# Optimization experiments

Measured on AMD Instinct MI355X. Metric: run time of the kernel, lower is better.

Reference implementation:

```python
import jax, jax.numpy as jnp
import numpy as np
from jax import lax

ALPHA = 0.5       # voxel vs structure weighting
BETA = 0.5        # split vs merge weighting
THRESHOLD = 0.0   # logit threshold for binarizing predictions
N_ITERS = 48      # label-propagation + pointer-jumping rounds (effective reach ~2^N)


def _shift(x, axis, s):
    """Shift x by s along axis, zero-filling the boundary (labels are >= 0)."""
    pads = [(0, 0)] * x.ndim
    pads[axis] = (max(s, 0), max(-s, 0))
    xp = jnp.pad(x, pads)
    idx = [slice(None)] * x.ndim
    idx[axis] = slice(max(-s, 0), max(-s, 0) + x.shape[axis])
    return xp[tuple(idx)]


def label_ccl(mask):
    """Connected-component labeling of a 3D boolean mask with 6-connectivity
    (scipy.ndimage.label default structure). Each component ends up holding the
    max linear index (+1) of its voxels; background is 0. Uses max-propagation
    over the 6-neighborhood plus pointer jumping for fast convergence."""
    size = mask.size
    ids = jnp.arange(1, size + 1, dtype=jnp.int32).reshape(mask.shape)
    lbl0 = jnp.where(mask, ids, 0)

    def body(_, lbl):
        m = lbl
        for ax in range(3):
            for s in (1, -1):
                m = jnp.maximum(m, _shift(lbl, ax, s))
        m = jnp.where(mask, m, 0)
        # pointer jumping: look up the label stored at the voxel my label points to
        hop = m.ravel()[jnp.maximum(m - 1, 0)]
        return jnp.where(mask, jnp.maximum(m, hop), 0)

    return lax.fori_loop(0, N_ITERS, body, lbl0)


def detect_critical(labels, other_fg):
    """Mark every connected component of `labels` that is not fully covered by
    the other segmentation's foreground (i.e., contains at least one mistake);
    the whole component is flagged as a structure-level (critical) error."""
    size = labels.size
    err = (labels > 0) & (~other_fg)
    has_err = jax.ops.segment_max(
        err.ravel().astype(jnp.int32), labels.ravel(), num_segments=size + 1
    )
    return ((has_err[labels] > 0) & (labels > 0)).astype(jnp.float32)


def setup_inputs() -> dict:
    key = jax.random.key(0)
    k1, k2 = jax.random.split(key)
    preds = jax.random.normal(k1, (2, 2, 128, 128, 128), dtype=jnp.float32)
    targets = jax.random.randint(k2, (2, 1, 128, 128, 128), 0, 2, dtype=jnp.int32)
    return {"preds": preds, "targets": targets}


def reference(preds, targets):
    # per-voxel robust cross entropy (reduction='none') over the 2-class channel dim
    tgt = targets[:, 0].astype(jnp.int32)                      # (B, D, H, W)
    logp = jax.nn.log_softmax(preds, axis=1)                   # (B, 2, D, H, W)
    loss = -jnp.take_along_axis(logp, tgt[:, None], axis=1)[:, 0]  # (B, D, H, W)

    # binarize and label both segmentations (apply_nonlin=None -> raw logits)
    pred_fg = preds[:, 1] > THRESHOLD
    tgt_fg = tgt > 0
    pred_lbl = jax.vmap(label_ccl)(pred_fg)
    tgt_lbl = jax.vmap(label_ccl)(tgt_fg)

    # critical_type=-1 (pred vs target components) scaled by beta,
    # critical_type=+1 (target vs pred components) scaled by (1 - beta)
    m_neg = jax.vmap(detect_critical)(tgt_lbl, pred_fg)
    m_pos = jax.vmap(detect_critical)(pred_lbl, tgt_fg)
    crit = BETA * m_neg + (1.0 - BETA) * m_pos

    # blend voxel-level and structure-level loss, then mean over the batch
    loss = (1.0 - ALPHA) * loss + ALPHA * crit * loss
    return loss.mean()
```

## Files before the change

### kernel.cpp

```cpp
#include <hip/hip_runtime.h>
#include <math.h>

#define VOL   (128 * 128 * 128)
#define NB    2
#define TOTAL (NB * VOL)

#define INVP   0x7FFFFFFFu
#define FLAGB  0x80000000u
#define IDXM   0x7FFFFFFFu
#define LINV   0xFFFFFFFFu

#define TPV            (8 * 8 * 8)
#define FACES_PER_DIR  (7 * 8 * 8)
#define FACES_PER_VOL  (3 * FACES_PER_DIR)
#define NFACES         (NB * FACES_PER_VOL)

__device__ __forceinline__ unsigned find_root(unsigned* P, unsigned i) {
    while (true) {
        unsigned p = P[i] & IDXM;
        if (p == i) return i;
        unsigned gp = P[p] & IDXM;
        if (gp != p) atomicMin(&P[i], gp);
        i = gp;
    }
}

__device__ __forceinline__ void unite(unsigned* P, unsigned a, unsigned b) {
    a = find_root(P, a);
    b = find_root(P, b);
    while (a != b) {
        if (b > a) { unsigned t = a; a = b; b = t; }
        unsigned old = atomicMin(&P[a], b);
        if (old == a) return;
        a = find_root(P, old & IDXM);
        b = find_root(P, b);
    }
}

__device__ __forceinline__ unsigned lfind(unsigned* L, unsigned i) {
    while (true) {
        unsigned p = L[i];
        if (p == i) return i;
        unsigned gp = L[p];
        if (gp != p) atomicMin(&L[i], gp);
        i = gp;
    }
}

__device__ __forceinline__ void lunite(unsigned* L, unsigned a, unsigned b) {
    a = lfind(L, a);
    b = lfind(L, b);
    while (a != b) {
        if (b > a) { unsigned t = a; a = b; b = t; }
        unsigned old = atomicMin(&L[a], b);
        if (old == a) return;
        a = lfind(L, old);
        b = lfind(L, b);
    }
}


__global__ void k_zero(unsigned* __restrict__ cnts) {
    if (threadIdx.x < 4) cnts[threadIdx.x] = 0;
}

__global__ void k_local(const float* __restrict__ preds,
                        const int* __restrict__ tgt,
                        unsigned* __restrict__ Pp,
                        unsigned* __restrict__ Pt,
                        unsigned* __restrict__ listP,
                        unsigned* __restrict__ listT,
                        unsigned* __restrict__ cnts,
                        unsigned cap) {
    __shared__ unsigned lpp[4096], lpt[4096];
    __shared__ unsigned perr[128], terr[128];
    __shared__ unsigned s_scan[256];
    __shared__ unsigned s_gbase;
    unsigned tile = blockIdx.x;
    unsigned b  = tile >> 9;
    unsigned tz = (tile >> 6) & 7, ty = (tile >> 3) & 7, tx = tile & 7;
    unsigned base_v = tz * (16 * 16384) + ty * (16 * 128) + tx * 16;
    unsigned base_g = b * VOL + base_v;

    if (threadIdx.x < 128) { perr[threadIdx.x] = 0; terr[threadIdx.x] = 0; }
    for (int l = threadIdx.x; l < 4096; l += 256) {
        unsigned lx = l & 15, ly = (l >> 4) & 15, lz = l >> 8;
        unsigned voli = base_v + lz * 16384 + ly * 128 + lx;
        float p1 = preds[(size_t)(b * 2 + 1) * VOL + voli];
        int   t  = tgt[b * VOL + voli];
        lpp[l] = (p1 > 0.0f) ? (unsigned)l : LINV;
        lpt[l] = (t > 0)     ? (unsigned)l : LINV;
    }
    __syncthreads();

    for (int l = threadIdx.x; l < 4096; l += 256) {
        unsigned lx = l & 15, ly = (l >> 4) & 15, lz = l >> 8;
        if (lpp[l] != LINV) {
            if (lx < 15 && lpp[l + 1]   != LINV) lunite(lpp, l, l + 1);
            if (ly < 15 && lpp[l + 16]  != LINV) lunite(lpp, l, l + 16);
            if (lz < 15 && lpp[l + 256] != LINV) lunite(lpp, l, l + 256);
        }
        if (lpt[l] != LINV) {
            if (lx < 15 && lpt[l + 1]   != LINV) lunite(lpt, l, l + 1);
            if (ly < 15 && lpt[l + 16]  != LINV) lunite(lpt, l, l + 16);
            if (lz < 15 && lpt[l + 256] != LINV) lunite(lpt, l, l + 256);
        }
    }
    __syncthreads();

    for (int l = threadIdx.x; l < 4096; l += 256) {
        unsigned lx = l & 15, ly = (l >> 4) & 15, lz = l >> 8;
        unsigned g = base_g + lz * 16384 + ly * 128 + lx;
        bool pf = lpp[l] != LINV, tf = lpt[l] != LINV;
        if (pf) {
            unsigned r = lfind(lpp, l);
            Pp[g] = base_g + (r >> 8) * 16384 + ((r >> 4) & 15) * 128 + (r & 15);
            if (!tf) atomicOr(&perr[r >> 5], 1u << (r & 31));
        } else Pp[g] = INVP;
        if (tf) {
            unsigned r = lfind(lpt, l);
            Pt[g] = base_g + (r >> 8) * 16384 + ((r >> 4) & 15) * 128 + (r & 15);
            if (!pf) atomicOr(&terr[r >> 5], 1u << (r & 31));
        } else Pt[g] = INVP;
    }
    __syncthreads();

    for (int arr = 0; arr < 2; ++arr) {
        unsigned* L  = arr ? lpt : lpp;
        unsigned* EB = arr ? terr : perr;
        unsigned* list = arr ? listT : listP;
        unsigned myCnt = 0;
        for (int k = 0; k < 16; ++k) {
            int l = threadIdx.x + k * 256;
            if (L[l] == (unsigned)l) myCnt++;
        }
        s_scan[threadIdx.x] = myCnt;
        __syncthreads();
        for (int off = 1; off < 256; off <<= 1) {
            unsigned v = (threadIdx.x >= (unsigned)off) ? s_scan[threadIdx.x - off] : 0u;
            __syncthreads();
            s_scan[threadIdx.x] += v;
            __syncthreads();
        }
        if (threadIdx.x == 255) s_gbase = atomicAdd(&cnts[arr], s_scan[255]);
        unsigned mybase = s_scan[threadIdx.x] - myCnt;
        __syncthreads();
        unsigned w = 0;
        for (int k = 0; k < 16; ++k) {
            int l = threadIdx.x + k * 256;
            if (L[l] == (unsigned)l) {
                unsigned idx = s_gbase + mybase + (w++);
                if (idx < cap) {
                    unsigned gid = base_g + (l >> 8) * 16384 + ((l >> 4) & 15) * 128 + (l & 15);
                    unsigned eb = (EB[l >> 5] >> (l & 31)) & 1u;
                    list[idx] = gid | (eb ? FLAGB : 0u);
                }
            }
        }
        __syncthreads();
    }
}

__global__ void k_bmerge(unsigned* __restrict__ Pp, unsigned* __restrict__ Pt) {
    unsigned fid = blockIdx.x;
    unsigned vol = fid / FACES_PER_VOL;
    unsigned r   = fid % FACES_PER_VOL;
    unsigned dir = r / FACES_PER_DIR;
    unsigned fr  = r % FACES_PER_DIR;
    unsigned b0 = fr % 7;
    unsigned t1 = (fr / 7) % 8;
    unsigned t2 = fr / 56;
    unsigned u = threadIdx.x & 15, v = threadIdx.x >> 4;
    unsigned lane = threadIdx.x & 63;

    unsigned x, y, z, step;
    if (dir == 0)      { x = b0 * 16 + 15; y = t1 * 16 + u; z = t2 * 16 + v; step = 1; }
    else if (dir == 1) { y = b0 * 16 + 15; x = t1 * 16 + u; z = t2 * 16 + v; step = 128; }
    else               { z = b0 * 16 + 15; x = t1 * 16 + u; y = t2 * 16 + v; step = 16384; }
    unsigned g = vol * VOL + z * 16384 + y * 128 + x;

    for (int arr = 0; arr < 2; ++arr) {
        unsigned* P = arr ? Pt : Pp;
        unsigned a = P[g];
        unsigned bb = P[g + step];
        bool need = (a != INVP) && (bb != INVP);
        bool leader = false;
        unsigned long long rem = __ballot(need);
        while (rem) {
            int src = __ffsll(rem) - 1;
            unsigned sa = __shfl(a, src), sb = __shfl(bb, src);
            if (need && a == sa && bb == sb) {
                leader = ((int)lane == src);
                need = false;
            }
            rem = __ballot(need);
        }
        if (leader) unite(P, a, bb);
    }
}

__global__ void k_rcompress(unsigned* __restrict__ Pp, unsigned* __restrict__ Pt,
                            const unsigned* __restrict__ listP,
                            const unsigned* __restrict__ listT,
                            const unsigned* __restrict__ cnts, unsigned cap) {
    unsigned nP = cnts[0] < cap ? cnts[0] : cap;
    unsigned nT = cnts[1] < cap ? cnts[1] : cap;
    unsigned total = nP + nT;
    for (unsigned i = blockIdx.x * blockDim.x + threadIdx.x; i < total;
         i += gridDim.x * blockDim.x) {
        unsigned* P = (i < nP) ? Pp : Pt;
        unsigned e = (i < nP) ? listP[i] : listT[i - nP];
        unsigned r = e & IDXM;
        unsigned rt = find_root(P, r);
        if (rt != r) atomicMin(&P[r], rt);
        if ((e & FLAGB) && !(P[rt] & FLAGB)) atomicOr(&P[rt], FLAGB);
    }
}

__global__ void k_rpull(unsigned* __restrict__ Pp, unsigned* __restrict__ Pt,
                        const unsigned* __restrict__ listP,
                        const unsigned* __restrict__ listT,
                        const unsigned* __restrict__ cnts, unsigned cap) {
    unsigned nP = cnts[0] < cap ? cnts[0] : cap;
    unsigned nT = cnts[1] < cap ? cnts[1] : cap;
    unsigned total = nP + nT;
    for (unsigned i = blockIdx.x * blockDim.x + threadIdx.x; i < total;
         i += gridDim.x * blockDim.x) {
        unsigned* P = (i < nP) ? Pp : Pt;
        unsigned r = ((i < nP) ? listP[i] : listT[i - nP]) & IDXM;
        unsigned root = P[r] & IDXM;
        if ((P[root] & FLAGB) && !(P[r] & FLAGB)) atomicOr(&P[r], FLAGB);
    }
}

__global__ void k_loss(const float* __restrict__ preds,
                       const int* __restrict__ tgt,
                       const unsigned* __restrict__ Pp,
                       const unsigned* __restrict__ Pt,
                       float* __restrict__ partial) {
    float acc = 0.0f;
    for (unsigned g = blockIdx.x * blockDim.x + threadIdx.x; g < TOTAL;
         g += gridDim.x * blockDim.x) {
        unsigned b = g >> 21;
        unsigned i = g & (VOL - 1);
        float p0 = preds[((size_t)(b * 2 + 0)) * VOL + i];
        float p1 = preds[((size_t)(b * 2 + 1)) * VOL + i];
        int   t  = tgt[g];
        float z  = (t > 0) ? (p0 - p1) : (p1 - p0);
        float ce = (z > 0.0f) ? (z + log1pf(expf(-z))) : log1pf(expf(z));

        unsigned vp = Pp[g], vt = Pt[g];
        float crit = 0.0f;
        if (vt != INVP) {
            unsigned r = vt & IDXM;
            if (Pt[r] & FLAGB) crit += 0.5f;
        }
        if (vp != INVP) {
            unsigned r = vp & IDXM;
            if (Pp[r] & FLAGB) crit += 0.5f;
        }
        acc += 0.5f * ce * (1.0f + crit);
    }
    for (int off = 32; off > 0; off >>= 1) acc += __shfl_down(acc, off);
    __shared__ float s[4];
    int wid = threadIdx.x >> 6, lane = threadIdx.x & 63;
    if (lane == 0) s[wid] = acc;
    __syncthreads();
    if (threadIdx.x == 0) {
        float tacc = 0.0f;
        for (int w = 0; w < (int)(blockDim.x >> 6); ++w) tacc += s[w];
        partial[blockIdx.x] = tacc;
    }
}

__global__ void k_final(const float* __restrict__ partial, int n,
                        float* __restrict__ out) {
    double acc = 0.0;
    for (int i = threadIdx.x; i < n; i += blockDim.x) acc += (double)partial[i];
    for (int off = 32; off > 0; off >>= 1) acc += __shfl_down(acc, off);
    __shared__ double s[4];
    int wid = threadIdx.x >> 6, lane = threadIdx.x & 63;
    if (lane == 0) s[wid] = acc;
    __syncthreads();
    if (threadIdx.x == 0) {
        double t = 0.0;
        for (int w = 0; w < (int)(blockDim.x >> 6); ++w) t += s[w];
        out[0] = (float)(t / (double)TOTAL);
    }
}


extern "C" void kernel_launch(void* const* d_in, const int* in_sizes, int n_in,
                              void* d_out, int out_size, void* d_ws, size_t ws_size,
                              hipStream_t stream) {
    const float* preds   = (const float*)d_in[0];
    const int*   targets = (const int*)d_in[1];
    float*       out     = (float*)d_out;

    unsigned* Pp = (unsigned*)d_ws;
    unsigned* Pt = Pp + TOTAL;
    float* partial = (float*)(Pt + TOTAL);
    unsigned* cnts = (unsigned*)(partial + 2048);
    unsigned* listP = cnts + 4;
    size_t used = (size_t)((char*)listP - (char*)d_ws);
    size_t avail = ws_size > used ? ws_size - used : 0;
    size_t cap_sz = avail / 8;
    unsigned cap = cap_sz > 524288 ? 524288u : (unsigned)cap_sz;
    unsigned* listT = listP + cap;

    const int T = 256;
    const int NTILE = NB * TPV;
    k_zero     <<<1, 64, 0, stream>>>(cnts);
    k_local    <<<NTILE, T, 0, stream>>>(preds, targets, Pp, Pt, listP, listT, cnts, cap);
    k_bmerge   <<<NFACES, T, 0, stream>>>(Pp, Pt);
    k_rcompress<<<128, T, 0, stream>>>(Pp, Pt, listP, listT, cnts, cap);
    k_rpull    <<<128, T, 0, stream>>>(Pp, Pt, listP, listT, cnts, cap);

    const int RB = 2048;
    k_loss <<<RB, T, 0, stream>>>(preds, targets, Pp, Pt, partial);
    k_final<<<1, T, 0, stream>>>(partial, RB, out);
}
```

Measured before the change: 287.7 us.

## Vectorize tile and loss loads, merge root lists into one tagged list

The tile load in k_local and the main loop in k_loss now use float4/int4/uint4 loads, four voxels per thread. The two per-array root lists become one list, with a tag bit telling pred and target apart. This drops one prefix scan and its barriers in k_local, and lets the compress and pull passes share one loop. The aim is fewer memory transactions and less sync overhead, but global ids now have to fit in 30 bits and the per-list capacity logic changes.

Result: faster. 261.6 us (-9.1%).

```diff
diff --git a/kernel.cpp b/kernel.cpp
--- a/kernel.cpp
+++ b/kernel.cpp
@@ -7,6 +7,8 @@
 
 #define INVP   0x7FFFFFFFu
 #define FLAGB  0x80000000u
+#define TAGB   0x40000000u
+#define GIDM   0x3FFFFFFFu
 #define IDXM   0x7FFFFFFFu
 #define LINV   0xFFFFFFFFu
 
@@ -68,8 +70,7 @@
                         const int* __restrict__ tgt,
                         unsigned* __restrict__ Pp,
                         unsigned* __restrict__ Pt,
-                        unsigned* __restrict__ listP,
-                        unsigned* __restrict__ listT,
+                        unsigned* __restrict__ list,
                         unsigned* __restrict__ cnts,
                         unsigned cap) {
     __shared__ unsigned lpp[4096], lpt[4096];
@@ -83,13 +84,23 @@
     unsigned base_g = b * VOL + base_v;
 
     if (threadIdx.x < 128) { perr[threadIdx.x] = 0; terr[threadIdx.x] = 0; }
-    for (int l = threadIdx.x; l < 4096; l += 256) {
-        unsigned lx = l & 15, ly = (l >> 4) & 15, lz = l >> 8;
+    for (int base = threadIdx.x * 4; base < 4096; base += 1024) {
+        unsigned lx = base & 15, ly = (base >> 4) & 15, lz = base >> 8;
         unsigned voli = base_v + lz * 16384 + ly * 128 + lx;
-        float p1 = preds[(size_t)(b * 2 + 1) * VOL + voli];
-        int   t  = tgt[b * VOL + voli];
-        lpp[l] = (p1 > 0.0f) ? (unsigned)l : LINV;
-        lpt[l] = (t > 0)     ? (unsigned)l : LINV;
+        float4 p1 = *reinterpret_cast<const float4*>(
+            preds + (size_t)(b * 2 + 1) * VOL + voli);
+        int4  t4 = *reinterpret_cast<const int4*>(tgt + b * VOL + voli);
+        uint4 vp, vt;
+        vp.x = (p1.x > 0.0f) ? (unsigned)(base + 0) : LINV;
+        vp.y = (p1.y > 0.0f) ? (unsigned)(base + 1) : LINV;
+        vp.z = (p1.z > 0.0f) ? (unsigned)(base + 2) : LINV;
+        vp.w = (p1.w > 0.0f) ? (unsigned)(base + 3) : LINV;
+        vt.x = (t4.x > 0) ? (unsigned)(base + 0) : LINV;
+        vt.y = (t4.y > 0) ? (unsigned)(base + 1) : LINV;
+        vt.z = (t4.z > 0) ? (unsigned)(base + 2) : LINV;
+        vt.w = (t4.w > 0) ? (unsigned)(base + 3) : LINV;
+        *reinterpret_cast<uint4*>(&lpp[base]) = vp;
+        *reinterpret_cast<uint4*>(&lpt[base]) = vt;
     }
     __syncthreads();
 
@@ -125,39 +136,40 @@
     }
     __syncthreads();
 
-    for (int arr = 0; arr < 2; ++arr) {
-        unsigned* L  = arr ? lpt : lpp;
-        unsigned* EB = arr ? terr : perr;
-        unsigned* list = arr ? listT : listP;
-        unsigned myCnt = 0;
-        for (int k = 0; k < 16; ++k) {
-            int l = threadIdx.x + k * 256;
-            if (L[l] == (unsigned)l) myCnt++;
-        }
-        s_scan[threadIdx.x] = myCnt;
+    unsigned myCnt = 0;
+    for (int k = 0; k < 16; ++k) {
+        int l = threadIdx.x + k * 256;
+        myCnt += (lpp[l] == (unsigned)l) + (lpt[l] == (unsigned)l);
+    }
+    s_scan[threadIdx.x] = myCnt;
+    __syncthreads();
+    for (int off = 1; off < 256; off <<= 1) {
+        unsigned v = (threadIdx.x >= (unsigned)off) ? s_scan[threadIdx.x - off] : 0u;
         __syncthreads();
-        for (int off = 1; off < 256; off <<= 1) {
-            unsigned v = (threadIdx.x >= (unsigned)off) ? s_scan[threadIdx.x - off] : 0u;
-            __syncthreads();
-            s_scan[threadIdx.x] += v;
-            __syncthreads();
-        }
-        if (threadIdx.x == 255) s_gbase = atomicAdd(&cnts[arr], s_scan[255]);
-        unsigned mybase = s_scan[threadIdx.x] - myCnt;
+        s_scan[threadIdx.x] += v;
         __syncthreads();
-        unsigned w = 0;
-        for (int k = 0; k < 16; ++k) {
-            int l = threadIdx.x + k * 256;
-            if (L[l] == (unsigned)l) {
-                unsigned idx = s_gbase + mybase + (w++);
-                if (idx < cap) {
-                    unsigned gid = base_g + (l >> 8) * 16384 + ((l >> 4) & 15) * 128 + (l & 15);
-                    unsigned eb = (EB[l >> 5] >> (l & 31)) & 1u;
-                    list[idx] = gid | (eb ? FLAGB : 0u);
-                }
-            }
-        }
-        __syncthreads();
+    }
+    if (threadIdx.x == 255) s_gbase = atomicAdd(&cnts[0], s_scan[255]);
+    unsigned mybase = s_scan[threadIdx.x] - myCnt;
+    __syncthreads();
+    unsigned idx = s_gbase + mybase;
+    for (int k = 0; k < 16; ++k) {
+        int l = threadIdx.x + k * 256;
+        unsigned gid = base_g + (l >> 8) * 16384 + ((l >> 4) & 15) * 128 + (l & 15);
+        if (lpp[l] == (unsigned)l) {
+            if (idx < cap) {
+                unsigned eb = (perr[l >> 5] >> (l & 31)) & 1u;
+                list[idx] = gid | (eb ? FLAGB : 0u);
+            }
+            idx++;
+        }
+        if (lpt[l] == (unsigned)l) {
+            if (idx < cap) {
+                unsigned eb = (terr[l >> 5] >> (l & 31)) & 1u;
+                list[idx] = gid | TAGB | (eb ? FLAGB : 0u);
+            }
+            idx++;
+        }
     }
 }
 
@@ -200,17 +212,14 @@
 }
 
 __global__ void k_rcompress(unsigned* __restrict__ Pp, unsigned* __restrict__ Pt,
-                            const unsigned* __restrict__ listP,
-                            const unsigned* __restrict__ listT,
+                            const unsigned* __restrict__ list,
                             const unsigned* __restrict__ cnts, unsigned cap) {
-    unsigned nP = cnts[0] < cap ? cnts[0] : cap;
-    unsigned nT = cnts[1] < cap ? cnts[1] : cap;
-    unsigned total = nP + nT;
-    for (unsigned i = blockIdx.x * blockDim.x + threadIdx.x; i < total;
+    unsigned n = cnts[0] < cap ? cnts[0] : cap;
+    for (unsigned i = blockIdx.x * blockDim.x + threadIdx.x; i < n;
          i += gridDim.x * blockDim.x) {
-        unsigned* P = (i < nP) ? Pp : Pt;
-        unsigned e = (i < nP) ? listP[i] : listT[i - nP];
-        unsigned r = e & IDXM;
+        unsigned e = list[i];
+        unsigned* P = (e & TAGB) ? Pt : Pp;
+        unsigned r = e & GIDM;
         unsigned rt = find_root(P, r);
         if (rt != r) atomicMin(&P[r], rt);
         if ((e & FLAGB) && !(P[rt] & FLAGB)) atomicOr(&P[rt], FLAGB);
@@ -218,16 +227,14 @@
 }
 
 __global__ void k_rpull(unsigned* __restrict__ Pp, unsigned* __restrict__ Pt,
-                        const unsigned* __restrict__ listP,
-                        const unsigned* __restrict__ listT,
+                        const unsigned* __restrict__ list,
                         const unsigned* __restrict__ cnts, unsigned cap) {
-    unsigned nP = cnts[0] < cap ? cnts[0] : cap;
-    unsigned nT = cnts[1] < cap ? cnts[1] : cap;
-    unsigned total = nP + nT;
-    for (unsigned i = blockIdx.x * blockDim.x + threadIdx.x; i < total;
+    unsigned n = cnts[0] < cap ? cnts[0] : cap;
+    for (unsigned i = blockIdx.x * blockDim.x + threadIdx.x; i < n;
          i += gridDim.x * blockDim.x) {
-        unsigned* P = (i < nP) ? Pp : Pt;
-        unsigned r = ((i < nP) ? listP[i] : listT[i - nP]) & IDXM;
+        unsigned e = list[i];
+        unsigned* P = (e & TAGB) ? Pt : Pp;
+        unsigned r = e & GIDM;
         unsigned root = P[r] & IDXM;
         if ((P[root] & FLAGB) && !(P[r] & FLAGB)) atomicOr(&P[r], FLAGB);
     }
@@ -239,27 +246,35 @@
                        const unsigned* __restrict__ Pt,
                        float* __restrict__ partial) {
     float acc = 0.0f;
-    for (unsigned g = blockIdx.x * blockDim.x + threadIdx.x; g < TOTAL;
-         g += gridDim.x * blockDim.x) {
-        unsigned b = g >> 21;
-        unsigned i = g & (VOL - 1);
-        float p0 = preds[((size_t)(b * 2 + 0)) * VOL + i];
-        float p1 = preds[((size_t)(b * 2 + 1)) * VOL + i];
-        int   t  = tgt[g];
-        float z  = (t > 0) ? (p0 - p1) : (p1 - p0);
-        float ce = (z > 0.0f) ? (z + log1pf(expf(-z))) : log1pf(expf(z));
-
-        unsigned vp = Pp[g], vt = Pt[g];
-        float crit = 0.0f;
-        if (vt != INVP) {
-            unsigned r = vt & IDXM;
-            if (Pt[r] & FLAGB) crit += 0.5f;
-        }
-        if (vp != INVP) {
-            unsigned r = vp & IDXM;
-            if (Pp[r] & FLAGB) crit += 0.5f;
-        }
-        acc += 0.5f * ce * (1.0f + crit);
+    for (unsigned g4 = (blockIdx.x * blockDim.x + threadIdx.x) * 4; g4 < TOTAL;
+         g4 += gridDim.x * blockDim.x * 4) {
+        unsigned b = g4 >> 21;
+        unsigned i = g4 & (VOL - 1);
+        float4 p0 = *reinterpret_cast<const float4*>(preds + (size_t)(b * 2 + 0) * VOL + i);
+        float4 p1 = *reinterpret_cast<const float4*>(preds + (size_t)(b * 2 + 1) * VOL + i);
+        int4  t4  = *reinterpret_cast<const int4*>(tgt + g4);
+        uint4 vp4 = *reinterpret_cast<const uint4*>(Pp + g4);
+        uint4 vt4 = *reinterpret_cast<const uint4*>(Pt + g4);
+        float p0a[4] = {p0.x, p0.y, p0.z, p0.w};
+        float p1a[4] = {p1.x, p1.y, p1.z, p1.w};
+        int   ta[4]  = {t4.x, t4.y, t4.z, t4.w};
+        unsigned vpa[4] = {vp4.x, vp4.y, vp4.z, vp4.w};
+        unsigned vta[4] = {vt4.x, vt4.y, vt4.z, vt4.w};
+        #pragma unroll
+        for (int j = 0; j < 4; ++j) {
+            float z  = (ta[j] > 0) ? (p0a[j] - p1a[j]) : (p1a[j] - p0a[j]);
+            float ce = (z > 0.0f) ? (z + log1pf(expf(-z))) : log1pf(expf(z));
+            float crit = 0.0f;
+            if (vta[j] != INVP) {
+                unsigned r = vta[j] & IDXM;
+                if (Pt[r] & FLAGB) crit += 0.5f;
+            }
+            if (vpa[j] != INVP) {
+                unsigned r = vpa[j] & IDXM;
+                if (Pp[r] & FLAGB) crit += 0.5f;
+            }
+            acc += 0.5f * ce * (1.0f + crit);
+        }
     }
     for (int off = 32; off > 0; off >>= 1) acc += __shfl_down(acc, off);
     __shared__ float s[4];
@@ -301,20 +316,19 @@
     unsigned* Pt = Pp + TOTAL;
     float* partial = (float*)(Pt + TOTAL);
     unsigned* cnts = (unsigned*)(partial + 2048);
-    unsigned* listP = cnts + 4;
-    size_t used = (size_t)((char*)listP - (char*)d_ws);
+    unsigned* list = cnts + 4;
+    size_t used = (size_t)((char*)list - (char*)d_ws);
     size_t avail = ws_size > used ? ws_size - used : 0;
-    size_t cap_sz = avail / 8;
-    unsigned cap = cap_sz > 524288 ? 524288u : (unsigned)cap_sz;
-    unsigned* listT = listP + cap;
+    size_t cap_sz = avail / 4;
+    unsigned cap = cap_sz > 1048576 ? 1048576u : (unsigned)cap_sz;
 
     const int T = 256;
     const int NTILE = NB * TPV;
     k_zero     <<<1, 64, 0, stream>>>(cnts);
-    k_local    <<<NTILE, T, 0, stream>>>(preds, targets, Pp, Pt, listP, listT, cnts, cap);
+    k_local    <<<NTILE, T, 0, stream>>>(preds, targets, Pp, Pt, list, cnts, cap);
     k_bmerge   <<<NFACES, T, 0, stream>>>(Pp, Pt);
-    k_rcompress<<<128, T, 0, stream>>>(Pp, Pt, listP, listT, cnts, cap);
-    k_rpull    <<<128, T, 0, stream>>>(Pp, Pt, listP, listT, cnts, cap);
+    k_rcompress<<<128, T, 0, stream>>>(Pp, Pt, list, cnts, cap);
+    k_rpull    <<<128, T, 0, stream>>>(Pp, Pt, list, cnts, cap);
 
     const int RB = 2048;
     k_loss <<<RB, T, 0, stream>>>(preds, targets, Pp, Pt, partial);
```
